# Optimization experiments

Measured on AMD Instinct MI355X. Metric: run time of the kernel, lower is better.

The kernel has to match this reference:

```python
import jax, jax.numpy as jnp
import numpy as np
from jax import lax

B, C, H, W = 2, 256, 48, 48
NUM_HEADS = 8
HEAD_DIM = C // NUM_HEADS
SCALE = HEAD_DIM ** (-0.5)
K1, K2 = 2, 3


def avgpool_same(y, k, pad):
    # torch AvgPool2d(kernel=k, stride=1, padding=pad), count_include_pad=True
    s = lax.reduce_window(y, 0.0, lax.add, (1, 1, k, k), (1, 1, 1, 1),
                          [(0, 0), (0, 0), (pad, pad), (pad, pad)])
    return s / (k * k)


def setup_inputs() -> dict:
    key = jax.random.key(0)
    ks = jax.random.split(key, 8)
    x = jax.random.normal(ks[0], (B, C, H, W), dtype=jnp.float32)
    y = jax.random.normal(ks[1], (B, C, H, W), dtype=jnp.float32)
    w = 0.02
    Wq = jax.random.normal(ks[2], (C, C), dtype=jnp.float32) * w
    Wkv = jax.random.normal(ks[3], (C, 2 * C), dtype=jnp.float32) * w
    Wproj = jax.random.normal(ks[4], (C, C), dtype=jnp.float32) * w
    bproj = jnp.zeros((C,), dtype=jnp.float32)
    gamma = jnp.ones((C,), dtype=jnp.float32)
    beta = jnp.zeros((C,), dtype=jnp.float32)
    attn_w1 = jnp.array([0.5], dtype=jnp.float32)
    attn_w2 = jnp.array([0.5], dtype=jnp.float32)
    return {"x": x, "y": y, "Wq": Wq, "Wkv": Wkv, "Wproj": Wproj,
            "bproj": bproj, "gamma": gamma, "beta": beta,
            "attn_w1": attn_w1, "attn_w2": attn_w2}


def _topk_branch(attn, kcount, v):
    # scatter 1.0 at top-k indices, mask everything else to -inf, softmax, @ v
    _, idx = lax.top_k(attn, kcount)                       # [B,h,N,kcount]
    mask = jnp.zeros_like(attn)
    mask = jnp.put_along_axis(mask, idx, 1.0, axis=-1, inplace=False)
    a = jnp.where(mask > 0, attn, -jnp.inf)
    a = jax.nn.softmax(a, axis=-1)
    return jnp.einsum('bhnm,bhmd->bhnd', a, v)


def reference(x, y, Wq, Wkv, Wproj, bproj, gamma, beta, attn_w1, attn_w2):
    # multi-scale avg pooling on y (all size-preserving, stride 1)
    yp = avgpool_same(y, 3, 1) + avgpool_same(y, 5, 2) + avgpool_same(y, 7, 3)
    yt = yp.reshape(B, C, H * W).transpose(0, 2, 1)        # [B, N1, C]
    mu = jnp.mean(yt, axis=-1, keepdims=True)
    var = jnp.var(yt, axis=-1, keepdims=True)
    yt = (yt - mu) / jnp.sqrt(var + 1e-5) * gamma + beta

    xt = x.reshape(B, C, H * W).transpose(0, 2, 1)         # [B, N, C]
    N = H * W
    N1 = H * W

    kv = (yt @ Wkv).reshape(B, N1, 2, NUM_HEADS, HEAD_DIM).transpose(2, 0, 3, 1, 4)
    k, v = kv[0], kv[1]                                    # [B,h,N1,hd]
    q = (xt @ Wq).reshape(B, N, NUM_HEADS, HEAD_DIM).transpose(0, 2, 1, 3)

    attn = jnp.einsum('bhnd,bhmd->bhnm', q, k) * SCALE     # [B,h,N,N1]

    out1 = _topk_branch(attn, N1 // K1, v)
    out2 = _topk_branch(attn, N1 // K2, v)
    out = out1 * attn_w1[0] + out2 * attn_w2[0]            # [B,h,N,hd]

    out = out.transpose(0, 2, 1, 3).reshape(B, N, C)
    out = out @ Wproj + bproj
    return out.transpose(0, 2, 1).reshape(B, C, H, W)
```

## Files before the change

kernel.cpp:

```cpp
#include <hip/hip_runtime.h>

#define BB     2
#define CC     256
#define HH     48
#define WW     48
#define NTOK   2304
#define NHEADS 8
#define HDIM   32
#define NBH    16
#define SCALE_QK 0.17677669529663687f
#define KSEL1  1152
#define KSEL2  768
#define NBIN   512
#define GCAP   320
#define LOSCALE 2048.0f

typedef _Float16 f16x8 __attribute__((ext_vector_type(8)));
typedef float f32x4 __attribute__((ext_vector_type(4)));

__device__ __forceinline__ int binof(float v) {
  int b = (int)((v + 1.0f) * 256.0f);
  return min(max(b, 0), NBIN - 1);
}

__global__ __launch_bounds__(256) void pool_kernel(const float* __restrict__ y,
                                                   float* __restrict__ yp) {
  __shared__ float sp[HH * WW];
  __shared__ float I[49 * 49];
  const int bc = blockIdx.x;
  const float* src = y + (size_t)bc * (HH * WW);
  for (int i = threadIdx.x; i < HH * WW; i += 256) sp[i] = src[i];
  __syncthreads();
  if (threadIdx.x < 48) {
    int r = threadIdx.x;
    float acc = 0.f;
    I[(r + 1) * 49 + 0] = 0.f;
    for (int j = 0; j < 48; ++j) { acc += sp[r * 48 + j]; I[(r + 1) * 49 + j + 1] = acc; }
  } else if (threadIdx.x < 97) {
    int j = threadIdx.x - 48;
    I[j] = 0.f;
  }
  __syncthreads();
  if (threadIdx.x < 48) {
    int j = threadIdx.x + 1;
    float acc = 0.f;
    for (int i = 1; i <= 48; ++i) { acc += I[i * 49 + j]; I[i * 49 + j] = acc; }
  }
  __syncthreads();
  for (int n = threadIdx.x; n < HH * WW; n += 256) {
    int i = n / 48, j = n % 48;
    float r = 0.f;
#pragma unroll
    for (int kk = 0; kk < 3; ++kk) {
      int p = 1 + kk;
      int i0 = i - p; if (i0 < 0) i0 = 0;
      int j0 = j - p; if (j0 < 0) j0 = 0;
      int i1 = i + p + 1; if (i1 > 48) i1 = 48;
      int j1 = j + p + 1; if (j1 > 48) j1 = 48;
      float s = I[i1 * 49 + j1] - I[i0 * 49 + j1] - I[i1 * 49 + j0] + I[i0 * 49 + j0];
      int k = 2 * p + 1;
      r += s / (float)(k * k);
    }
    yp[(size_t)bc * (HH * WW) + n] = r;
  }
}

__global__ __launch_bounds__(256) void ln_kernel(const float* __restrict__ yp,
                                                 const float* __restrict__ gamma,
                                                 const float* __restrict__ beta,
                                                 _Float16* __restrict__ yth,
                                                 _Float16* __restrict__ ytl) {
  __shared__ float tile[CC][33];
  __shared__ float part[8][32];
  __shared__ float part2[8][32];
  const int b = blockIdx.y;
  const int n0 = blockIdx.x * 32;
  const int tid = threadIdx.x;
#pragma unroll
  for (int it = 0; it < 32; ++it) {
    int idx = it * 256 + tid;
    int c = idx >> 5, nl = idx & 31;
    tile[c][nl] = yp[((size_t)(b * CC + c)) * NTOK + n0 + nl];
  }
  __syncthreads();
  const int nl = tid & 31, cs = tid >> 5;
  float s = 0.f, s2 = 0.f;
#pragma unroll
  for (int i = 0; i < 32; ++i) {
    float v = tile[cs * 32 + i][nl];
    s += v; s2 += v * v;
  }
  part[cs][nl] = s; part2[cs][nl] = s2;
  __syncthreads();
  float S = 0.f, S2 = 0.f;
#pragma unroll
  for (int i = 0; i < 8; ++i) { S += part[i][nl]; S2 += part2[i][nl]; }
  const float mean = S * (1.f / CC);
  const float var = S2 * (1.f / CC) - mean * mean;
  const float rstd = rsqrtf(var + 1e-5f);
  const size_t dstb = ((size_t)(b * NTOK + n0 + nl)) * CC + cs * 32;
#pragma unroll
  for (int g8 = 0; g8 < 4; ++g8) {
    f16x8 vh, vl;
#pragma unroll
    for (int e = 0; e < 8; ++e) {
      int c = cs * 32 + g8 * 8 + e;
      float o = (tile[c][nl] - mean) * rstd * gamma[c] + beta[c];
      _Float16 hi = (_Float16)o;
      vh[e] = hi;
      vl[e] = (_Float16)((o - (float)hi) * LOSCALE);
    }
    *(f16x8*)(yth + dstb + g8 * 8) = vh;
    *(f16x8*)(ytl + dstb + g8 * 8) = vl;
  }
}

__global__ __launch_bounds__(256) void xcast_kernel(const float* __restrict__ x,
                                                    _Float16* __restrict__ xh,
                                                    _Float16* __restrict__ xl) {
  __shared__ float tile[64][65];
  const int b = blockIdx.z;
  const int nb = blockIdx.x;
  const int cb = blockIdx.y;
  const int tid = threadIdx.x;
#pragma unroll
  for (int it = 0; it < 16; ++it) {
    int idx = it * 256 + tid;
    int cl = idx >> 6, nl = idx & 63;
    tile[cl][nl] = x[((size_t)(b * CC + cb * 64 + cl)) * NTOK + nb * 64 + nl];
  }
  __syncthreads();
#pragma unroll
  for (int it = 0; it < 16; ++it) {
    int idx = it * 256 + tid;
    int nl = idx >> 6, cl = idx & 63;
    float v = tile[cl][nl];
    size_t dst = ((size_t)(b * NTOK + nb * 64 + nl)) * CC + cb * 64 + cl;
    _Float16 hi = (_Float16)v;
    xh[dst] = hi;
    xl[dst] = (_Float16)((v - (float)hi) * LOSCALE);
  }
}

__global__ __launch_bounds__(256) void wtcast3_kernel(
    const float* __restrict__ Wq, const float* __restrict__ Wkv,
    const float* __restrict__ Wproj,
    _Float16* __restrict__ wqh, _Float16* __restrict__ wql,
    _Float16* __restrict__ wkvh, _Float16* __restrict__ wkvl,
    _Float16* __restrict__ wph, _Float16* __restrict__ wpl) {
  const int blk = blockIdx.x;
  const int k = threadIdx.x;
  const float* W; _Float16 *wh, *wl; int ncol, col; float scale;
  if (blk < CC)            { W = Wq;    wh = wqh;  wl = wql;  ncol = CC;     col = blk;          scale = SCALE_QK; }
  else if (blk < 3 * CC)   { W = Wkv;   wh = wkvh; wl = wkvl; ncol = 2 * CC; col = blk - CC;     scale = 1.0f; }
  else                     { W = Wproj; wh = wph;  wl = wpl;  ncol = CC;     col = blk - 3 * CC; scale = 1.0f; }
  float v = W[(size_t)k * ncol + col] * scale;
  _Float16 hi = (_Float16)v;
  wh[(size_t)col * CC + k] = hi;
  wl[(size_t)col * CC + k] = (_Float16)((v - (float)hi) * LOSCALE);
}

template <int MODE>
__global__ __launch_bounds__(256) void gemm_hilo_kernel(
    const _Float16* __restrict__ Ah, const _Float16* __restrict__ Al,
    const float* __restrict__ Af,
    const _Float16* __restrict__ Bh, const _Float16* __restrict__ Bl,
    const float* __restrict__ bias,
    _Float16* __restrict__ Oh, _Float16* __restrict__ Ol,
    _Float16* __restrict__ Ov, float* __restrict__ Of) {
  const int w = threadIdx.x >> 6;
  const int lane = threadIdx.x & 63;
  const int wm = w >> 1, wc = w & 1;
  const int r16 = lane & 15, kg = lane >> 4;
  const int m0 = blockIdx.x * 64 + wm * 32;
  const int c0 = blockIdx.y * 64 + wc * 32;
  const f32x4 fz = {0.f, 0.f, 0.f, 0.f};
  f32x4 acc00 = fz, acc01 = fz, acc10 = fz, acc11 = fz;
  f32x4 ac200 = fz, ac201 = fz, ac210 = fz, ac211 = fz;
  for (int ks = 0; ks < CC; ks += 32) {
    f16x8 ah_[2], al_[2], bh_[2], bl_[2];
#pragma unroll
    for (int i = 0; i < 2; ++i) {
      size_t offa = (size_t)(m0 + i * 16 + r16) * CC + ks + kg * 8;
      if constexpr (MODE == 2) {
        f32x4 a0 = *(const f32x4*)(Af + offa);
        f32x4 a1 = *(const f32x4*)(Af + offa + 4);
#pragma unroll
        for (int e = 0; e < 4; ++e) {
          _Float16 h0 = (_Float16)a0[e];
          ah_[i][e] = h0;
          al_[i][e] = (_Float16)((a0[e] - (float)h0) * LOSCALE);
          _Float16 h1 = (_Float16)a1[e];
          ah_[i][e + 4] = h1;
          al_[i][e + 4] = (_Float16)((a1[e] - (float)h1) * LOSCALE);
        }
      } else {
        ah_[i] = *(const f16x8*)(Ah + offa);
        al_[i] = *(const f16x8*)(Al + offa);
      }
      size_t offb = (size_t)(c0 + i * 16 + r16) * CC + ks + kg * 8;
      bh_[i] = *(const f16x8*)(Bh + offb);
      bl_[i] = *(const f16x8*)(Bl + offb);
    }
    acc00 = __builtin_amdgcn_mfma_f32_16x16x32_f16(ah_[0], bh_[0], acc00, 0, 0, 0);
    ac200 = __builtin_amdgcn_mfma_f32_16x16x32_f16(ah_[0], bl_[0], ac200, 0, 0, 0);
    ac200 = __builtin_amdgcn_mfma_f32_16x16x32_f16(al_[0], bh_[0], ac200, 0, 0, 0);
    acc01 = __builtin_amdgcn_mfma_f32_16x16x32_f16(ah_[0], bh_[1], acc01, 0, 0, 0);
    ac201 = __builtin_amdgcn_mfma_f32_16x16x32_f16(ah_[0], bl_[1], ac201, 0, 0, 0);
    ac201 = __builtin_amdgcn_mfma_f32_16x16x32_f16(al_[0], bh_[1], ac201, 0, 0, 0);
    acc10 = __builtin_amdgcn_mfma_f32_16x16x32_f16(ah_[1], bh_[0], acc10, 0, 0, 0);
    ac210 = __builtin_amdgcn_mfma_f32_16x16x32_f16(ah_[1], bl_[0], ac210, 0, 0, 0);
    ac210 = __builtin_amdgcn_mfma_f32_16x16x32_f16(al_[1], bh_[0], ac210, 0, 0, 0);
    acc11 = __builtin_amdgcn_mfma_f32_16x16x32_f16(ah_[1], bh_[1], acc11, 0, 0, 0);
    ac211 = __builtin_amdgcn_mfma_f32_16x16x32_f16(ah_[1], bl_[1], ac211, 0, 0, 0);
    ac211 = __builtin_amdgcn_mfma_f32_16x16x32_f16(al_[1], bh_[1], ac211, 0, 0, 0);
  }
  f32x4 accs[2][2] = {{acc00, acc01}, {acc10, acc11}};
  f32x4 ac2s[2][2] = {{ac200, ac201}, {ac210, ac211}};
  if constexpr (MODE == 2) {
    __shared__ float ts[4][32][33];
#pragma unroll
    for (int i = 0; i < 2; ++i)
#pragma unroll
      for (int j = 0; j < 2; ++j)
#pragma unroll
        for (int r = 0; r < 4; ++r)
          ts[w][i * 16 + kg * 4 + r][j * 16 + r16] =
              accs[i][j][r] + ac2s[i][j][r] * (1.f / LOSCALE);
    __syncthreads();
    const int b = m0 / NTOK;
    const int n_base = m0 % NTOK;
#pragma unroll
    for (int t = 0; t < 16; ++t) {
      int idx = t * 64 + lane;
      int ml = idx & 31, cl = idx >> 5;
      float v = ts[w][ml][cl] + bias[c0 + cl];
      Of[((size_t)(b * CC + c0 + cl)) * NTOK + n_base + ml] = v;
    }
  } else {
#pragma unroll
    for (int i = 0; i < 2; ++i) {
#pragma unroll
      for (int j = 0; j < 2; ++j) {
#pragma unroll
        for (int r = 0; r < 4; ++r) {
          float val = accs[i][j][r] + ac2s[i][j][r] * (1.f / LOSCALE);
          int m = m0 + i * 16 + kg * 4 + r;
          int c = c0 + j * 16 + r16;
          int b = m / NTOK, n = m % NTOK;
          if (MODE == 0 || c < CC) {
            int h = (c & (CC - 1)) >> 5, d = c & 31;
            size_t dst = ((size_t)((b * 8 + h) * NTOK) + n) * HDIM + d;
            _Float16 hi = (_Float16)val;
            Oh[dst] = hi;
            Ol[dst] = (_Float16)((val - (float)hi) * LOSCALE);
          } else {
            int cc2 = c - CC;
            int h2 = cc2 >> 5, d2 = cc2 & 31;
            Ov[((size_t)((b * NHEADS + h2) * HDIM + d2)) * NTOK + n] = (_Float16)val;
          }
        }
      }
    }
  }
}

#define SMSTEP 4
__global__ __launch_bounds__(256) void score_mfma_kernel(const _Float16* __restrict__ qh,
                                                         const _Float16* __restrict__ ql,
                                                         const _Float16* __restrict__ kh,
                                                         const _Float16* __restrict__ kl,
                                                         _Float16* __restrict__ sc, int bh0) {
  const int w = threadIdx.x >> 6;
  const int lane = threadIdx.x & 63;
  const int wn = w >> 1, wm = w & 1;
  const int r16 = lane & 15, kg = lane >> 4;
  const int z = blockIdx.z;
  const int gbh = bh0 + z;
  const size_t tb = (size_t)gbh * NTOK * HDIM;
  const int n0 = blockIdx.x * 64 + wn * 32;
  const f32x4 fz = {0.f, 0.f, 0.f, 0.f};
  f16x8 ah[2], al[2];
#pragma unroll
  for (int i = 0; i < 2; ++i) {
    size_t off = tb + (size_t)(n0 + i * 16 + r16) * HDIM + kg * 8;
    ah[i] = *(const f16x8*)(qh + off);
    al[i] = *(const f16x8*)(ql + off);
  }
  for (int s = 0; s < SMSTEP; ++s) {
    const int ms = blockIdx.y * (SMSTEP * 64) + s * 64 + wm * 32;
    f16x8 bhf[2], blf[2];
#pragma unroll
    for (int j = 0; j < 2; ++j) {
      size_t off = tb + (size_t)(ms + j * 16 + r16) * HDIM + kg * 8;
      bhf[j] = *(const f16x8*)(kh + off);
      blf[j] = *(const f16x8*)(kl + off);
    }
#pragma unroll
    for (int i = 0; i < 2; ++i)
#pragma unroll
      for (int j = 0; j < 2; ++j) {
        f32x4 acc = __builtin_amdgcn_mfma_f32_16x16x32_f16(ah[i], bhf[j], fz, 0, 0, 0);
        f32x4 ac2 = __builtin_amdgcn_mfma_f32_16x16x32_f16(ah[i], blf[j], fz, 0, 0, 0);
        ac2 = __builtin_amdgcn_mfma_f32_16x16x32_f16(al[i], bhf[j], ac2, 0, 0, 0);
        size_t rowbase = ((size_t)z * NTOK + n0 + i * 16 + kg * 4) * NTOK + ms + j * 16 + r16;
#pragma unroll
        for (int r = 0; r < 4; ++r)
          sc[rowbase + (size_t)r * NTOK] = (_Float16)(acc[r] + ac2[r] * (1.0f / LOSCALE));
      }
  }
}

template <int NPL>
__device__ __forceinline__ void radix_find(const unsigned* __restrict__ h,
                                           unsigned krem, unsigned* sres2) {
  const int lane = threadIdx.x & 63;
  unsigned c[NPL];
#pragma unroll
  for (int i = 0; i < NPL; ++i) c[i] = h[lane * NPL + i];
  unsigned suf[NPL];
  unsigned run = 0;
#pragma unroll
  for (int i = NPL - 1; i >= 0; --i) { run += c[i]; suf[i] = run; }
  unsigned acc = run;
#pragma unroll
  for (int off = 1; off < 64; off <<= 1) {
    unsigned t = __shfl_down(acc, off);
    if (lane + off < 64) acc += t;
  }
  unsigned tail = __shfl_down(acc, 1);
  if (lane == 63) tail = 0;
#pragma unroll
  for (int i = 0; i < NPL; ++i) {
    unsigned s = tail + suf[i];
    unsigned nx = (i + 1 < NPL) ? (tail + suf[i + 1]) : tail;
    if (s >= krem && nx < krem) {
      sres2[0] = (unsigned)(lane * NPL + i);
      sres2[1] = krem - nx;
    }
  }
}

__global__ __launch_bounds__(256) void select_kernel(const _Float16* __restrict__ sc,
                                                     float* __restrict__ stats,
                                                     const float* __restrict__ w1p,
                                                     const float* __restrict__ w2p) {
  __shared__ unsigned cnt[NBIN];
  __shared__ float buf[2][GCAP];
  __shared__ unsigned bcnt[2];
  __shared__ unsigned sres[4];
  __shared__ float tthr[2];
  __shared__ float psw[4];
  const int tid = threadIdx.x;
  const int wv = tid >> 6, lane = tid & 63;
  const size_t base = (size_t)blockIdx.x * NTOK;
  for (int i = tid; i < NBIN; i += 256) cnt[i] = 0u;
  if (tid < 2) bcnt[tid] = 0u;
  __syncthreads();
  const bool two = (tid < (NTOK / 8 - 256));
  f16x8 r0 = *((const f16x8*)(sc + base) + tid);
  f16x8 r1 = two ? *((const f16x8*)(sc + base) + 256 + tid) : f16x8{};
#pragma unroll
  for (int e = 0; e < 8; ++e) atomicAdd(&cnt[binof((float)r0[e])], 1u);
  if (two) {
#pragma unroll
    for (int e = 0; e < 8; ++e) atomicAdd(&cnt[binof((float)r1[e])], 1u);
  }
  __syncthreads();
  if (tid < 64)       radix_find<NBIN / 64>(cnt, KSEL1, &sres[0]);
  else if (tid < 128) radix_find<NBIN / 64>(cnt, KSEL2, &sres[2]);
  __syncthreads();
  const int b1 = (int)sres[0], b2 = (int)sres[2];
  const unsigned k1 = sres[1], k2 = sres[3];
  const unsigned c1 = cnt[b1], c2 = cnt[b2];
  const bool g1ok = (c1 <= GCAP), g2ok = (c2 <= GCAP);
  const float lo1 = (b1 == 0) ? -3.4e38f : ((float)b1 * (1.f / 256.f) - 1.f);
  const float hi1 = (b1 == NBIN - 1) ? 3.4e38f : ((float)(b1 + 1) * (1.f / 256.f) - 1.f);
  const float lo2 = (b2 == 0) ? -3.4e38f : ((float)b2 * (1.f / 256.f) - 1.f);
  const float hi2 = (b2 == NBIN - 1) ? 3.4e38f : ((float)(b2 + 1) * (1.f / 256.f) - 1.f);
#pragma unroll
  for (int e = 0; e < 8; ++e) {
    float v = (float)r0[e];
    if (g1ok && v >= lo1 && v < hi1) buf[0][atomicAdd(&bcnt[0], 1u)] = v;
    if (g2ok && v >= lo2 && v < hi2) buf[1][atomicAdd(&bcnt[1], 1u)] = v;
  }
  if (two) {
#pragma unroll
    for (int e = 0; e < 8; ++e) {
      float v = (float)r1[e];
      if (g1ok && v >= lo1 && v < hi1) buf[0][atomicAdd(&bcnt[0], 1u)] = v;
      if (g2ok && v >= lo2 && v < hi2) buf[1][atomicAdd(&bcnt[1], 1u)] = v;
    }
  }
  __syncthreads();
  {
    const int sel = wv & 1, half = wv >> 1;
    const unsigned kk = sel ? k2 : k1;
    const int bb = sel ? b2 : b1;
    const unsigned cc = sel ? c2 : c1;
    if (cc <= GCAP) {
      for (unsigned i = half * 64 + lane; i < cc; i += 128) {
        float xv = buf[sel][i];
        unsigned g = 0, m = 0;
        for (unsigned j2 = 0; j2 < cc; ++j2) {
          float yv = buf[sel][j2];
          g += (yv > xv) ? 1u : 0u;
          m += (yv == xv) ? 1u : 0u;
        }
        if (g < kk && kk <= g + m) tthr[sel] = xv;
      }
    } else if (half == 0) {
      for (int i = lane; i < NTOK; i += 64) {
        float xv = (float)sc[base + i];
        if (binof(xv) != bb) continue;
        unsigned g = 0, m = 0;
        for (int j2 = 0; j2 < NTOK; ++j2) {
          float yv = (float)sc[base + j2];
          if (binof(yv) != bb) continue;
          g += (yv > xv) ? 1u : 0u;
          m += (yv == xv) ? 1u : 0u;
        }
        if (g < kk && kk <= g + m) tthr[sel] = xv;
      }
    }
  }
  __syncthreads();
  {
    const int sel = wv & 1, half = wv >> 1;
    const int bb = sel ? b2 : b1;
    const unsigned cc = sel ? c2 : c1;
    const float t = tthr[sel];
    float ps = 0.f;
    if (cc <= GCAP) {
      for (unsigned i = half * 64 + lane; i < cc; i += 128) {
        float xv = buf[sel][i];
        if (xv >= t) ps += __expf(xv);
      }
    } else if (half == 0) {
      for (int i = lane; i < NTOK; i += 64) {
        float xv = (float)sc[base + i];
        if (binof(xv) == bb && xv >= t) ps += __expf(xv);
      }
    }
    for (int b = bb + 1 + half * 64 + lane; b < NBIN; b += 128)
      ps += (float)cnt[b] * __expf((float)b * (1.f / 256.f) + (0.5f / 256.f) - 1.f);
#pragma unroll
    for (int off = 32; off; off >>= 1) ps += __shfl_down(ps, off);
    if (lane == 0) psw[wv] = ps;
  }
  __syncthreads();
  if (tid == 0) {
    float D1 = psw[0] + psw[2];
    float D2 = psw[1] + psw[3];
    float* st = stats + (size_t)blockIdx.x * 8;
    st[0] = 0.f;
    st[1] = tthr[0];
    st[2] = tthr[1];
    st[3] = w1p[0] / D1;
    st[4] = w2p[0] / D2;
  }
}

#define MSPLIT 4
__global__ __launch_bounds__(256) void pv_mfma_kernel(const _Float16* __restrict__ sc,
                                                      const _Float16* __restrict__ vtb,
                                                      const float* __restrict__ stats,
                                                      float* __restrict__ oat, int bh0) {
  const int w = threadIdx.x >> 6;
  const int l = threadIdx.x & 63;
  const int z = blockIdx.z;
  const int gbh = bh0 + z;
  const int b = gbh >> 3, h = gbh & 7;
  const int n0 = blockIdx.x * 64 + w * 16;
  const int row = l & 15;
  const int kg = l >> 4;
  const int n = n0 + row;
  const float* st = stats + ((size_t)z * NTOK + n) * 8;
  const float mx = st[0], t1 = st[1], t2 = st[2], w1d = st[3], w2d = st[4];
  const _Float16* srow = sc + ((size_t)z * NTOK + n) * NTOK;
  const _Float16* v0 = vtb + ((size_t)gbh * HDIM + row) * NTOK;
  const _Float16* v1 = v0 + 16 * NTOK;
  f32x4 acc0 = {0.f, 0.f, 0.f, 0.f};
  f32x4 acc1 = {0.f, 0.f, 0.f, 0.f};
  const int msteps = (NTOK / 32) / MSPLIT;
  int m0 = blockIdx.y * msteps * 32 + kg * 8;
#pragma unroll 2
  for (int s = 0; s < msteps; ++s, m0 += 32) {
    f16x8 sv8 = *(const f16x8*)(srow + m0);
    f16x8 afr;
#pragma unroll
    for (int i = 0; i < 8; ++i) {
      float sv = (float)sv8[i];
      float e = __expf(sv - mx);
      float wgt = (sv >= t1 ? w1d : 0.f) + (sv >= t2 ? w2d : 0.f);
      afr[i] = (_Float16)(e * wgt);
    }
    f16x8 bfr0 = *(const f16x8*)(v0 + m0);
    f16x8 bfr1 = *(const f16x8*)(v1 + m0);
    acc0 = __builtin_amdgcn_mfma_f32_16x16x32_f16(afr, bfr0, acc0, 0, 0, 0);
    acc1 = __builtin_amdgcn_mfma_f32_16x16x32_f16(afr, bfr1, acc1, 0, 0, 0);
  }
#pragma unroll
  for (int r = 0; r < 4; ++r) {
    int nn = n0 + kg * 4 + r;
    float* dst = &oat[((size_t)(b * NTOK + nn)) * CC + h * HDIM];
    atomicAdd(&dst[row], acc0[r]);
    atomicAdd(&dst[16 + row], acc1[r]);
  }
}

extern "C" void kernel_launch(void* const* d_in, const int* in_sizes, int n_in,
                              void* d_out, int out_size, void* d_ws, size_t ws_size,
                              hipStream_t stream) {
  const float* x     = (const float*)d_in[0];
  const float* y     = (const float*)d_in[1];
  const float* Wq    = (const float*)d_in[2];
  const float* Wkv   = (const float*)d_in[3];
  const float* Wproj = (const float*)d_in[4];
  const float* bproj = (const float*)d_in[5];
  const float* gamma = (const float*)d_in[6];
  const float* beta  = (const float*)d_in[7];
  const float* aw1   = (const float*)d_in[8];
  const float* aw2   = (const float*)d_in[9];

  float* ws = (float*)d_ws;
  const size_t SZ_PLANE = (size_t)BB * CC * NTOK;
  const size_t SZ_TBL = (size_t)NBH * NTOK * HDIM;
  float* yp    = ws;
  float* oat   = yp + SZ_PLANE;
  float* stats = oat + SZ_PLANE;
  _Float16* yth = (_Float16*)(stats + (size_t)NBH * NTOK * 8);
  _Float16* ytl = yth + SZ_PLANE;
  _Float16* xh  = ytl + SZ_PLANE;
  _Float16* xl  = xh + SZ_PLANE;
  _Float16* wqh = xl + SZ_PLANE;
  _Float16* wql = wqh + CC * CC;
  _Float16* wkvh = wql + CC * CC;
  _Float16* wkvl = wkvh + 2 * CC * CC;
  _Float16* wph = wkvl + 2 * CC * CC;
  _Float16* wpl = wph + CC * CC;
  _Float16* qh  = wpl + CC * CC;
  _Float16* ql  = qh + SZ_TBL;
  _Float16* kh  = ql + SZ_TBL;
  _Float16* kl  = kh + SZ_TBL;
  _Float16* vtb = kl + SZ_TBL;
  _Float16* sc  = vtb + SZ_TBL;

  const long long fixed_f = (long long)((float*)sc - ws);
  const long long avail_f = (long long)(ws_size / 4) - fixed_f;
  int CH = 8;
  while (CH > 1 && (long long)CH * NTOK * NTOK / 2 > avail_f) CH >>= 1;

  pool_kernel<<<dim3(BB * CC), 256, 0, stream>>>(y, yp);
  ln_kernel<<<dim3(NTOK / 32, BB), 256, 0, stream>>>(yp, gamma, beta, yth, ytl);
  xcast_kernel<<<dim3(NTOK / 64, CC / 64, BB), 256, 0, stream>>>(x, xh, xl);
  wtcast3_kernel<<<dim3(4 * CC), 256, 0, stream>>>(Wq, Wkv, Wproj, wqh, wql,
                                                   wkvh, wkvl, wph, wpl);
  gemm_hilo_kernel<0><<<dim3(BB * NTOK / 64, CC / 64), 256, 0, stream>>>(
      xh, xl, nullptr, wqh, wql, nullptr, qh, ql, nullptr, nullptr);
  gemm_hilo_kernel<1><<<dim3(BB * NTOK / 64, 2 * CC / 64), 256, 0, stream>>>(
      yth, ytl, nullptr, wkvh, wkvl, nullptr, kh, kl, vtb, nullptr);

  hipMemsetAsync(oat, 0, SZ_PLANE * sizeof(float), stream);

  const int nch = NBH / CH;
  for (int ch = 0; ch < nch; ++ch) {
    int bh0 = ch * CH;
    score_mfma_kernel<<<dim3(NTOK / 64, NTOK / (SMSTEP * 64), CH), 256, 0, stream>>>(
        qh, ql, kh, kl, sc, bh0);
    select_kernel<<<dim3(CH * NTOK), 256, 0, stream>>>(sc, stats, aw1, aw2);
    pv_mfma_kernel<<<dim3(NTOK / 64, MSPLIT, CH), 256, 0, stream>>>(sc, vtb, stats, oat, bh0);
  }

  gemm_hilo_kernel<2><<<dim3(BB * NTOK / 64, CC / 64), 256, 0, stream>>>(
      nullptr, nullptr, oat, wph, wpl, bproj, nullptr, nullptr, nullptr, (float*)d_out);
}
```

Before: 336.6 us.

## Process one score row per wavefront in top-k select kernel

The select kernel now gives each wavefront its own attention row, with a private histogram, candidate buffers and thresholds, instead of having the whole 256-thread block cooperate on one row. Block-wide __syncthreads are replaced by wave-local LDS waitcnt fences, and the grid shrinks by four. This is meant to remove block-level synchronisation and the cross-wave reduction. The candidate buffer capacity is reduced so that four copies fit in LDS, which sends more rows down the slow fallback path that rescans global memory.

```diff
diff --git a/kernel.cpp b/kernel.cpp
--- a/kernel.cpp
+++ b/kernel.cpp
@@ -12,7 +12,7 @@
 #define KSEL1  1152
 #define KSEL2  768
 #define NBIN   512
-#define GCAP   320
+#define GCAP   192
 #define LOSCALE 2048.0f
 
 typedef _Float16 f16x8 __attribute__((ext_vector_type(8)));
@@ -21,6 +21,12 @@
 __device__ __forceinline__ int binof(float v) {
   int b = (int)((v + 1.0f) * 256.0f);
   return min(max(b, 0), NBIN - 1);
+}
+
+__device__ __forceinline__ void wave_lds_fence() {
+  __builtin_amdgcn_sched_barrier(0);
+  asm volatile("s_waitcnt lgkmcnt(0)" ::: "memory");
+  __builtin_amdgcn_sched_barrier(0);
 }
 
 __global__ __launch_bounds__(256) void pool_kernel(const float* __restrict__ y,
@@ -345,71 +351,79 @@
                                                      float* __restrict__ stats,
                                                      const float* __restrict__ w1p,
                                                      const float* __restrict__ w2p) {
-  __shared__ unsigned cnt[NBIN];
-  __shared__ float buf[2][GCAP];
-  __shared__ unsigned bcnt[2];
-  __shared__ unsigned sres[4];
-  __shared__ float tthr[2];
-  __shared__ float psw[4];
+  __shared__ unsigned cnt[4][NBIN];
+  __shared__ float buf[4][2][GCAP];
+  __shared__ unsigned bcnt[4][2];
+  __shared__ unsigned sres[4][4];
+  __shared__ float tthr[4][2];
   const int tid = threadIdx.x;
   const int wv = tid >> 6, lane = tid & 63;
-  const size_t base = (size_t)blockIdx.x * NTOK;
-  for (int i = tid; i < NBIN; i += 256) cnt[i] = 0u;
-  if (tid < 2) bcnt[tid] = 0u;
-  __syncthreads();
-  const bool two = (tid < (NTOK / 8 - 256));
-  f16x8 r0 = *((const f16x8*)(sc + base) + tid);
-  f16x8 r1 = two ? *((const f16x8*)(sc + base) + 256 + tid) : f16x8{};
-#pragma unroll
-  for (int e = 0; e < 8; ++e) atomicAdd(&cnt[binof((float)r0[e])], 1u);
+  const int row = blockIdx.x * 4 + wv;
+  const size_t base = (size_t)row * NTOK;
+  unsigned* mycnt = cnt[wv];
+#pragma unroll
+  for (int i = 0; i < NBIN / 64; ++i) mycnt[lane * (NBIN / 64) + i] = 0u;
+  if (lane < 2) bcnt[wv][lane] = 0u;
+  wave_lds_fence();
+  f16x8 r[4];
+#pragma unroll
+  for (int j = 0; j < 4; ++j) r[j] = *((const f16x8*)(sc + base) + j * 64 + lane);
+  const bool two = (lane < 32);
+  f16x8 r4 = two ? *((const f16x8*)(sc + base) + 256 + lane) : f16x8{};
+#pragma unroll
+  for (int j = 0; j < 4; ++j)
+#pragma unroll
+    for (int e = 0; e < 8; ++e) atomicAdd(&mycnt[binof((float)r[j][e])], 1u);
   if (two) {
 #pragma unroll
-    for (int e = 0; e < 8; ++e) atomicAdd(&cnt[binof((float)r1[e])], 1u);
-  }
-  __syncthreads();
-  if (tid < 64)       radix_find<NBIN / 64>(cnt, KSEL1, &sres[0]);
-  else if (tid < 128) radix_find<NBIN / 64>(cnt, KSEL2, &sres[2]);
-  __syncthreads();
-  const int b1 = (int)sres[0], b2 = (int)sres[2];
-  const unsigned k1 = sres[1], k2 = sres[3];
-  const unsigned c1 = cnt[b1], c2 = cnt[b2];
+    for (int e = 0; e < 8; ++e) atomicAdd(&mycnt[binof((float)r4[e])], 1u);
+  }
+  wave_lds_fence();
+  radix_find<NBIN / 64>(mycnt, KSEL1, &sres[wv][0]);
+  radix_find<NBIN / 64>(mycnt, KSEL2, &sres[wv][2]);
+  wave_lds_fence();
+  const int b1 = (int)sres[wv][0], b2 = (int)sres[wv][2];
+  const unsigned k1 = sres[wv][1], k2 = sres[wv][3];
+  const unsigned c1 = mycnt[b1], c2 = mycnt[b2];
   const bool g1ok = (c1 <= GCAP), g2ok = (c2 <= GCAP);
   const float lo1 = (b1 == 0) ? -3.4e38f : ((float)b1 * (1.f / 256.f) - 1.f);
   const float hi1 = (b1 == NBIN - 1) ? 3.4e38f : ((float)(b1 + 1) * (1.f / 256.f) - 1.f);
   const float lo2 = (b2 == 0) ? -3.4e38f : ((float)b2 * (1.f / 256.f) - 1.f);
   const float hi2 = (b2 == NBIN - 1) ? 3.4e38f : ((float)(b2 + 1) * (1.f / 256.f) - 1.f);
 #pragma unroll
-  for (int e = 0; e < 8; ++e) {
-    float v = (float)r0[e];
-    if (g1ok && v >= lo1 && v < hi1) buf[0][atomicAdd(&bcnt[0], 1u)] = v;
-    if (g2ok && v >= lo2 && v < hi2) buf[1][atomicAdd(&bcnt[1], 1u)] = v;
-  }
+  for (int j = 0; j < 4; ++j)
+#pragma unroll
+    for (int e = 0; e < 8; ++e) {
+      float v = (float)r[j][e];
+      if (g1ok && v >= lo1 && v < hi1) buf[wv][0][atomicAdd(&bcnt[wv][0], 1u)] = v;
+      if (g2ok && v >= lo2 && v < hi2) buf[wv][1][atomicAdd(&bcnt[wv][1], 1u)] = v;
+    }
   if (two) {
 #pragma unroll
     for (int e = 0; e < 8; ++e) {
-      float v = (float)r1[e];
-      if (g1ok && v >= lo1 && v < hi1) buf[0][atomicAdd(&bcnt[0], 1u)] = v;
-      if (g2ok && v >= lo2 && v < hi2) buf[1][atomicAdd(&bcnt[1], 1u)] = v;
-    }
-  }
-  __syncthreads();
-  {
-    const int sel = wv & 1, half = wv >> 1;
+      float v = (float)r4[e];
+      if (g1ok && v >= lo1 && v < hi1) buf[wv][0][atomicAdd(&bcnt[wv][0], 1u)] = v;
+      if (g2ok && v >= lo2 && v < hi2) buf[wv][1][atomicAdd(&bcnt[wv][1], 1u)] = v;
+    }
+  }
+  wave_lds_fence();
+#pragma unroll
+  for (int sel = 0; sel < 2; ++sel) {
     const unsigned kk = sel ? k2 : k1;
     const int bb = sel ? b2 : b1;
     const unsigned cc = sel ? c2 : c1;
     if (cc <= GCAP) {
-      for (unsigned i = half * 64 + lane; i < cc; i += 128) {
-        float xv = buf[sel][i];
+      for (unsigned i = lane; i < cc; i += 64) {
+        float xv = buf[wv][sel][i];
         unsigned g = 0, m = 0;
         for (unsigned j2 = 0; j2 < cc; ++j2) {
-          float yv = buf[sel][j2];
+          float yv = buf[wv][sel][j2];
           g += (yv > xv) ? 1u : 0u;
           m += (yv == xv) ? 1u : 0u;
         }
-        if (g < kk && kk <= g + m) tthr[sel] = xv;
-      }
-    } else if (half == 0) {
+        if (g < kk && kk <= g + m) tthr[wv][sel] = xv;
+      }
+    } else {
       for (int i = lane; i < NTOK; i += 64) {
         float xv = (float)sc[base + i];
         if (binof(xv) != bb) continue;
@@ -420,44 +434,42 @@
           g += (yv > xv) ? 1u : 0u;
           m += (yv == xv) ? 1u : 0u;
         }
-        if (g < kk && kk <= g + m) tthr[sel] = xv;
-      }
-    }
-  }
-  __syncthreads();
-  {
-    const int sel = wv & 1, half = wv >> 1;
+        if (g < kk && kk <= g + m) tthr[wv][sel] = xv;
+      }
+    }
+  }
+  wave_lds_fence();
+  float D[2];
+#pragma unroll
+  for (int sel = 0; sel < 2; ++sel) {
     const int bb = sel ? b2 : b1;
     const unsigned cc = sel ? c2 : c1;
-    const float t = tthr[sel];
+    const float t = tthr[wv][sel];
     float ps = 0.f;
     if (cc <= GCAP) {
-      for (unsigned i = half * 64 + lane; i < cc; i += 128) {
-        float xv = buf[sel][i];
+      for (unsigned i = lane; i < cc; i += 64) {
+        float xv = buf[wv][sel][i];
         if (xv >= t) ps += __expf(xv);
       }
-    } else if (half == 0) {
+    } else {
       for (int i = lane; i < NTOK; i += 64) {
         float xv = (float)sc[base + i];
         if (binof(xv) == bb && xv >= t) ps += __expf(xv);
       }
     }
-    for (int b = bb + 1 + half * 64 + lane; b < NBIN; b += 128)
-      ps += (float)cnt[b] * __expf((float)b * (1.f / 256.f) + (0.5f / 256.f) - 1.f);
+    for (int b = bb + 1 + lane; b < NBIN; b += 64)
+      ps += (float)mycnt[b] * __expf((float)b * (1.f / 256.f) + (0.5f / 256.f) - 1.f);
 #pragma unroll
     for (int off = 32; off; off >>= 1) ps += __shfl_down(ps, off);
-    if (lane == 0) psw[wv] = ps;
-  }
-  __syncthreads();
-  if (tid == 0) {
-    float D1 = psw[0] + psw[2];
-    float D2 = psw[1] + psw[3];
-    float* st = stats + (size_t)blockIdx.x * 8;
+    D[sel] = ps;
+  }
+  if (lane == 0) {
+    float* st = stats + (size_t)row * 8;
     st[0] = 0.f;
-    st[1] = tthr[0];
-    st[2] = tthr[1];
-    st[3] = w1p[0] / D1;
-    st[4] = w2p[0] / D2;
+    st[1] = tthr[wv][0];
+    st[2] = tthr[wv][1];
+    st[3] = w1p[0] / D[0];
+    st[4] = w2p[0] / D[1];
   }
 }
 
@@ -568,7 +580,7 @@
     int bh0 = ch * CH;
     score_mfma_kernel<<<dim3(NTOK / 64, NTOK / (SMSTEP * 64), CH), 256, 0, stream>>>(
         qh, ql, kh, kl, sc, bh0);
-    select_kernel<<<dim3(CH * NTOK), 256, 0, stream>>>(sc, stats, aw1, aw2);
+    select_kernel<<<dim3(CH * NTOK / 4), 256, 0, stream>>>(sc, stats, aw1, aw2);
     pv_mfma_kernel<<<dim3(NTOK / 64, MSPLIT, CH), 256, 0, stream>>>(sc, vtb, stats, oat, bh0);
   }
 
```

Result: faster. 304.4 us (-9.6%).
